# Performance work log

Hardware: AMD Instinct MI355X
Metric: run time of the kernel (lower is better)

## Reference

```python
import jax, jax.numpy as jnp
import numpy as np

N_NODES = 50000
N_EDGES = 800000
IN_C, HID_C, OUT_C = 128, 128, 64
BN_EPS = 1e-5


def setup_inputs() -> dict:
    key = jax.random.key(0)
    ks = jax.random.split(key, 12)
    def lin(k, fan_in, fan_out):
        bound = 1.0 / np.sqrt(fan_in)
        kw, kb = jax.random.split(k)
        W = jax.random.uniform(kw, (fan_in, fan_out), jnp.float32, -bound, bound)
        b = jax.random.uniform(kb, (fan_out,), jnp.float32, -bound, bound)
        return W, b
    x = jax.random.normal(ks[0], (N_NODES, IN_C), jnp.float32)
    edge_index = jax.random.randint(ks[1], (2, N_EDGES), 0, N_NODES, jnp.int32)
    w1a, b1a = lin(ks[2], IN_C, HID_C)
    w1b, b1b = lin(ks[3], HID_C, HID_C)
    w2a, b2a = lin(ks[4], HID_C, OUT_C)
    w2b, b2b = lin(ks[5], OUT_C, OUT_C)
    return {
        "x": x, "edge_index": edge_index,
        "w1a": w1a, "b1a": b1a, "g1": jnp.ones((HID_C,)), "be1": jnp.zeros((HID_C,)),
        "w1b": w1b, "b1b": b1b,
        "w2a": w2a, "b2a": b2a, "g2": jnp.ones((OUT_C,)), "be2": jnp.zeros((OUT_C,)),
        "w2b": w2b, "b2b": b2b,
    }


def _batchnorm(h, gamma, beta):
    # training-style BN over node dim, biased variance (torch BatchNorm1d)
    mean = jnp.mean(h, axis=0)
    var = jnp.mean(jnp.square(h - mean), axis=0)
    return (h - mean) * jax.lax.rsqrt(var + BN_EPS) * gamma + beta


def _gin_layer(x, src, dst, n_nodes, w_a, b_a, gamma, beta, w_b, b_b):
    # GINConv with eps=0: MLP(x + sum_{j->i} x_j)
    agg = jax.ops.segment_sum(x[src], dst, num_segments=n_nodes)  # [N, C]
    h = x + agg
    h = h @ w_a + b_a
    h = jax.nn.relu(_batchnorm(h, gamma, beta))
    return h @ w_b + b_b


def reference(x, edge_index, w1a, b1a, g1, be1, w1b, b1b, w2a, b2a, g2, be2, w2b, b2b):
    src, dst = edge_index[0], edge_index[1]
    n = x.shape[0]
    h = _gin_layer(x, src, dst, n, w1a, b1a, g1, be1, w1b, b1b)
    h = jax.nn.relu(h)  # dropout p=0.0 -> identity
    h = _gin_layer(h, src, dst, n, w2a, b2a, g2, be2, w2b, b2b)
    return jax.nn.log_softmax(h, axis=-1)
```

## Files before the change

kernel.cpp:

```cpp
#include <hip/hip_runtime.h>


typedef unsigned short u16;
typedef unsigned int u32;
typedef __attribute__((ext_vector_type(8))) short short8;
typedef __attribute__((ext_vector_type(4))) short short4v;
typedef __attribute__((ext_vector_type(4))) float f32x4;

#define DEV_INLINE __device__ __forceinline__

DEV_INLINE void atomAddF(float* p, float v) { unsafeAtomicAdd(p, v); }

DEV_INLINE u16 f2bf(float f) {
    unsigned u = __float_as_uint(f);
    u += 0x7fffu + ((u >> 16) & 1u);
    return (u16)(u >> 16);
}
DEV_INLINE float bf2f(u16 h) { return __uint_as_float(((unsigned)h) << 16); }

__global__ __launch_bounds__(256) void wprep4_k(
    const float* __restrict__ w1a, const float* __restrict__ w1b,
    const float* __restrict__ w2a, const float* __restrict__ w2b,
    short* __restrict__ o1a, short* __restrict__ o1b,
    short* __restrict__ o2a, short* __restrict__ o2b)
{
    int b = blockIdx.x;
    const float* W; short* wf; int K, NOUT;
    if (b < 8)       { W = w1a; wf = o1a; K = 128; NOUT = 128; }
    else if (b < 16) { W = w1b; wf = o1b; K = 128; NOUT = 128; b -= 8; }
    else if (b < 20) { W = w2a; wf = o2a; K = 128; NOUT = 64;  b -= 16; }
    else             { W = w2b; wf = o2b; K = 64;  NOUT = 64;  b -= 20; }
    const int u = b * 256 + threadIdx.x;
    const int units = (NOUT / 16) * (K / 32) * 64;
    if (u >= units) return;
    const int per_ct = (K / 32) * 64;
    const int ct = u / per_ct;
    const int rem = u % per_ct;
    const int kc = rem >> 6;
    const int l = rem & 63;
    const int col = ct * 16 + (l & 15);
    const int k0 = kc * 32 + (l >> 4) * 8;
    short8 pk;
#pragma unroll
    for (int j = 0; j < 8; j++)
        pk[j] = (short)f2bf(W[(size_t)(k0 + j) * NOUT + col]);
    *(short8*)&wf[(size_t)u * 8] = pk;
}

template <int KD, int NC, bool ABF16, bool BNIN, bool BIAS, bool RELUOUT,
          bool LOGSM, bool OBF16>
__global__ __launch_bounds__(256) void mgemm(
    const void* __restrict__ Ap, const short* __restrict__ Wf,
    const float* __restrict__ sc, const float* __restrict__ sh,
    const float* __restrict__ bias, void* __restrict__ outp, int M)
{
    constexpr int BM = 128;
    constexpr int KC = KD / 32;
    constexpr int CT = NC / 16;
    __shared__ short Asl[BM * KD];
    __shared__ short Bsl[NC * KD];

    const int t = threadIdx.x;
    const int l = t & 63;
    const int w = t >> 6;

    {
        const float4* src = (const float4*)Wf;
        float4* dst = (float4*)Bsl;
        constexpr int NU = NC * KD / 8;
#pragma unroll
        for (int u = t; u < NU; u += 256) dst[u] = src[u];
    }
    {
        const int r = t >> 1;
        const int half = t & 1;
        const int grow = blockIdx.x * BM + r;
        const int rt = r >> 4;
        constexpr int KH = KD / 2;
        u16 hv[KH];
        if (grow < M) {
            if constexpr (ABF16) {
                const u16* ap = (const u16*)Ap + (size_t)grow * KD + half * KH;
#pragma unroll
                for (int i = 0; i < KH / 8; i++)
                    *(short8*)&hv[i * 8] = ((const short8*)ap)[i];
                if constexpr (BNIN) {
#pragma unroll
                    for (int i = 0; i < KH; i++) {
                        const int k = half * KH + i;
                        hv[i] = f2bf(fmaxf(0.f, bf2f(hv[i]) * sc[k] + sh[k]));
                    }
                }
            } else {
                const float* ap = (const float*)Ap + (size_t)grow * KD + half * KH;
#pragma unroll
                for (int i = 0; i < KH / 4; i++) {
                    const float4 v = ((const float4*)ap)[i];
                    float f0 = v.x, f1 = v.y, f2 = v.z, f3 = v.w;
                    if constexpr (BNIN) {
                        const int k = half * KH + i * 4;
                        f0 = fmaxf(0.f, f0 * sc[k + 0] + sh[k + 0]);
                        f1 = fmaxf(0.f, f1 * sc[k + 1] + sh[k + 1]);
                        f2 = fmaxf(0.f, f2 * sc[k + 2] + sh[k + 2]);
                        f3 = fmaxf(0.f, f3 * sc[k + 3] + sh[k + 3]);
                    }
                    hv[i * 4 + 0] = f2bf(f0); hv[i * 4 + 1] = f2bf(f1);
                    hv[i * 4 + 2] = f2bf(f2); hv[i * 4 + 3] = f2bf(f3);
                }
            }
        } else {
#pragma unroll
            for (int i = 0; i < KH; i++) hv[i] = 0;
        }
#pragma unroll
        for (int g = 0; g < KH / 8; g++) {
            const int k0 = half * KH + g * 8;
            const int kc = k0 >> 5;
            const int lane = (r & 15) + ((k0 >> 3) & 3) * 16;
            *(short8*)&Asl[((rt * KC + kc) * 64 + lane) * 8] =
                *(short8*)&hv[g * 8];
        }
    }
    __syncthreads();

    const int rt0 = w * 2;
    f32x4 acc[2][CT];
#pragma unroll
    for (int i = 0; i < 2; i++)
#pragma unroll
        for (int c = 0; c < CT; c++) acc[i][c] = (f32x4){0.f, 0.f, 0.f, 0.f};

#pragma unroll
    for (int kc = 0; kc < KC; kc++) {
        const short8 x0 = *(const short8*)&Asl[((rt0 * KC + kc) * 64 + l) * 8];
        const short8 x1 = *(const short8*)&Asl[(((rt0 + 1) * KC + kc) * 64 + l) * 8];
#pragma unroll
        for (int ct = 0; ct < CT; ct++) {
            const short8 wb = *(const short8*)&Bsl[((ct * KC + kc) * 64 + l) * 8];
            acc[0][ct] = __builtin_amdgcn_mfma_f32_16x16x32_bf16(wb, x0, acc[0][ct], 0, 0, 0);
            acc[1][ct] = __builtin_amdgcn_mfma_f32_16x16x32_bf16(wb, x1, acc[1][ct], 0, 0, 0);
        }
    }

    const int cbase = (l >> 4) * 4;
#pragma unroll
    for (int rr = 0; rr < 2; rr++) {
        const int grow = blockIdx.x * BM + (rt0 + rr) * 16 + (l & 15);
        if constexpr (!LOGSM) {
            if (grow < M) {
#pragma unroll
                for (int ct = 0; ct < CT; ct++) {
                    f32x4 o = acc[rr][ct];
                    if constexpr (BIAS) {
                        const float4 bv = *(const float4*)&bias[ct * 16 + cbase];
                        o[0] += bv.x; o[1] += bv.y; o[2] += bv.z; o[3] += bv.w;
                    }
                    if constexpr (RELUOUT) {
#pragma unroll
                        for (int j = 0; j < 4; j++) o[j] = fmaxf(o[j], 0.f);
                    }
                    if constexpr (OBF16) {
                        short4v o16;
#pragma unroll
                        for (int j = 0; j < 4; j++) o16[j] = (short)f2bf(o[j]);
                        *(short4v*)&((u16*)outp)[(size_t)grow * NC + ct * 16 + cbase] = o16;
                    } else {
                        *(f32x4*)&((float*)outp)[(size_t)grow * NC + ct * 16 + cbase] = o;
                    }
                }
            }
        } else {
            float v[CT * 4];
#pragma unroll
            for (int ct = 0; ct < CT; ct++) {
                const float4 bv = *(const float4*)&bias[ct * 16 + cbase];
                v[ct * 4 + 0] = acc[rr][ct][0] + bv.x;
                v[ct * 4 + 1] = acc[rr][ct][1] + bv.y;
                v[ct * 4 + 2] = acc[rr][ct][2] + bv.z;
                v[ct * 4 + 3] = acc[rr][ct][3] + bv.w;
            }
            float m = v[0];
#pragma unroll
            for (int j = 1; j < CT * 4; j++) m = fmaxf(m, v[j]);
            m = fmaxf(m, __shfl_xor(m, 16));
            m = fmaxf(m, __shfl_xor(m, 32));
            float s = 0.f;
#pragma unroll
            for (int j = 0; j < CT * 4; j++) s += __expf(v[j] - m);
            s += __shfl_xor(s, 16);
            s += __shfl_xor(s, 32);
            const float lg = m + __logf(s);
            if (grow < M) {
#pragma unroll
                for (int ct = 0; ct < CT; ct++) {
                    f32x4 o;
#pragma unroll
                    for (int j = 0; j < 4; j++) o[j] = v[ct * 4 + j] - lg;
                    *(f32x4*)&((float*)outp)[(size_t)grow * NC + ct * 16 + cbase] = o;
                }
            }
        }
    }
}

__global__ __launch_bounds__(256) void hist_k(const int* __restrict__ ei,
                                              int* __restrict__ cnt, int E)
{
    const int gid = blockIdx.x * blockDim.x + threadIdx.x;
    const int stride = gridDim.x * blockDim.x;
    for (int e = gid; e < E; e += stride) atomicAdd(&cnt[ei[E + e]], 1);
}

__global__ __launch_bounds__(256) void bsum_k(const int* __restrict__ cnt,
                                              int* __restrict__ bsum, int N)
{
    __shared__ int ws[4];
    const int i = blockIdx.x * 256 + threadIdx.x;
    int v = (i < N) ? cnt[i] : 0;
    for (int d = 32; d; d >>= 1) v += __shfl_xor(v, d, 64);
    if ((threadIdx.x & 63) == 0) ws[threadIdx.x >> 6] = v;
    __syncthreads();
    if (threadIdx.x == 0) bsum[blockIdx.x] = ws[0] + ws[1] + ws[2] + ws[3];
}

__global__ __launch_bounds__(256) void bscan_k(const int* __restrict__ bsum,
                                               int* __restrict__ bpre, int G1)
{
    __shared__ int part[256];
    const int t = threadIdx.x;
    const int v = (t < G1) ? bsum[t] : 0;
    part[t] = v;
    __syncthreads();
    for (int d = 1; d < 256; d <<= 1) {
        const int u = (t >= d) ? part[t - d] : 0;
        __syncthreads();
        part[t] += u;
        __syncthreads();
    }
    bpre[t] = part[t] - v;
}

__global__ __launch_bounds__(256) void offs_k(const int* __restrict__ cnt,
                                              const int* __restrict__ bpre,
                                              int* __restrict__ off,
                                              int* __restrict__ cursor,
                                              int N, int E)
{
    __shared__ int part[256];
    const int t = threadIdx.x;
    const int i = blockIdx.x * 256 + t;
    const int v = (i < N) ? cnt[i] : 0;
    part[t] = v;
    __syncthreads();
    for (int d = 1; d < 256; d <<= 1) {
        const int u = (t >= d) ? part[t - d] : 0;
        __syncthreads();
        part[t] += u;
        __syncthreads();
    }
    if (i < N) {
        const int o = bpre[blockIdx.x] + part[t] - v;
        off[i] = o;
        cursor[i] = o;
    }
    if (blockIdx.x == 0 && t == 0) off[N] = E;
}

__global__ __launch_bounds__(256) void fill_k(const int* __restrict__ ei,
                                              int* __restrict__ cursor,
                                              int* __restrict__ srcs, int E)
{
    const int gid = blockIdx.x * blockDim.x + threadIdx.x;
    const int stride = gridDim.x * blockDim.x;
    for (int e = gid; e < E; e += stride) {
        const int s = ei[e];
        const int d = ei[E + e];
        const int pos = atomicAdd(&cursor[d], 1);
        srcs[pos] = s;
    }
}

template <int C>
__global__ __launch_bounds__(256) void segsum_bf(
    const u16* __restrict__ p, const int* __restrict__ off,
    const int* __restrict__ srcs, u16* __restrict__ out,
    float* __restrict__ sum, float* __restrict__ sumsq, int N)
{
    constexpr int BLKN = 8;
    constexpr int VPL = C / 64;
    __shared__ float red[4][64][2 * VPL];

    const int wv = threadIdx.x >> 6;
    const int l  = threadIdx.x & 63;
    const int base = blockIdx.x * 4 * BLKN;

    float ss[VPL], qq[VPL];
#pragma unroll
    for (int v = 0; v < VPL; v++) { ss[v] = 0.f; qq[v] = 0.f; }

    for (int i = 0; i < BLKN; i++) {
        const int n = base + i * 4 + wv;
        if (n < N) {
            const int lo = __builtin_amdgcn_readfirstlane(off[n]);
            const int hi = __builtin_amdgcn_readfirstlane(off[n + 1]);
            float acc[VPL];
            if constexpr (VPL == 2) {
                const u32 u = *(const u32*)&p[(size_t)n * C + 2 * l];
                acc[0] = bf2f((u16)u);
                acc[1] = bf2f((u16)(u >> 16));
            } else {
                acc[0] = bf2f(p[(size_t)n * C + l]);
            }
            const int cnt = hi - lo;
            if (cnt > 0) {
                const int last = hi - 1;
                int idx[8];
#pragma unroll
                for (int j = 0; j < 8; j++) idx[j] = srcs[min(lo + j, last)];
                for (int e = lo; e < hi; e += 8) {
                    int nx[8];
#pragma unroll
                    for (int j = 0; j < 8; j++)
                        nx[j] = srcs[min(e + 8 + j, last)];
#pragma unroll
                    for (int j = 0; j < 8; j++) {
                        const bool live = (e + j) < hi;
                        if constexpr (VPL == 2) {
                            const u32 u = *(const u32*)&p[(size_t)idx[j] * C + 2 * l];
                            const float v0 = bf2f((u16)u);
                            const float v1 = bf2f((u16)(u >> 16));
                            acc[0] += live ? v0 : 0.f;
                            acc[1] += live ? v1 : 0.f;
                        } else {
                            const float v = bf2f(p[(size_t)idx[j] * C + l]);
                            acc[0] += live ? v : 0.f;
                        }
                    }
#pragma unroll
                    for (int j = 0; j < 8; j++) idx[j] = nx[j];
                }
            }
            if constexpr (VPL == 2) {
                const u16 r0 = f2bf(acc[0]);
                const u16 r1 = f2bf(acc[1]);
                *(u32*)&out[(size_t)n * C + 2 * l] = (u32)r0 | ((u32)r1 << 16);
                const float f0 = bf2f(r0), f1 = bf2f(r1);
                ss[0] += f0; qq[0] += f0 * f0;
                ss[1] += f1; qq[1] += f1 * f1;
            } else {
                const u16 r = f2bf(acc[0]);
                out[(size_t)n * C + l] = r;
                const float f = bf2f(r);
                ss[0] += f; qq[0] += f * f;
            }
        }
    }

#pragma unroll
    for (int v = 0; v < VPL; v++) {
        red[wv][l][2 * v] = ss[v];
        red[wv][l][2 * v + 1] = qq[v];
    }
    __syncthreads();
    if (wv == 0) {
#pragma unroll
        for (int v = 0; v < VPL; v++) {
            float a = 0.f, b = 0.f;
#pragma unroll
            for (int w2 = 0; w2 < 4; w2++) {
                a += red[w2][l][2 * v];
                b += red[w2][l][2 * v + 1];
            }
            const int ch = (VPL == 2) ? (2 * l + v) : l;
            atomAddF(&sum[ch], a);
            atomAddF(&sumsq[ch], b);
        }
    }
}

__global__ void bnfinal_k(const float* __restrict__ sum,
                          const float* __restrict__ sumsq,
                          const float* __restrict__ g,
                          const float* __restrict__ be,
                          float* __restrict__ sc, float* __restrict__ sh,
                          int C, float invN)
{
    const int c = threadIdx.x;
    if (c < C) {
        const float m = sum[c] * invN;
        const float v = sumsq[c] * invN - m * m;
        const float r = rsqrtf(v + 1e-5f);
        const float s = g[c] * r;
        sc[c] = s;
        sh[c] = be[c] - m * s;
    }
}

extern "C" void kernel_launch(void* const* d_in, const int* in_sizes, int n_in,
                              void* d_out, int out_size, void* d_ws, size_t ws_size,
                              hipStream_t stream)
{
    const float* x   = (const float*)d_in[0];
    const int*   ei  = (const int*)d_in[1];
    const float* w1a = (const float*)d_in[2];
    const float* g1  = (const float*)d_in[4];
    const float* be1 = (const float*)d_in[5];
    const float* w1b = (const float*)d_in[6];
    const float* b1b = (const float*)d_in[7];
    const float* w2a = (const float*)d_in[8];
    const float* g2  = (const float*)d_in[10];
    const float* be2 = (const float*)d_in[11];
    const float* w2b = (const float*)d_in[12];
    const float* b2b = (const float*)d_in[13];
    float* out = (float*)d_out;

    const int N = in_sizes[0] / 128;
    const int E = in_sizes[1] / 2;

    u16* buf1 = (u16*)d_ws;
    u16* buf2 = buf1 + (size_t)N * 128;
    float* stats = (float*)(buf2 + (size_t)N * 128);
    float* sum1 = stats,       *sq1 = stats + 128;
    float* sum2 = stats + 256, *sq2 = stats + 320;
    float* sc1  = stats + 384, *sh1 = stats + 512;
    float* sc2  = stats + 640, *sh2 = stats + 704;
    int* cnt    = (int*)(stats + 1024);
    int* off    = cnt + N;
    int* cursor = off + N + 1;
    int* srcs   = cursor + N;
    int* bsum   = srcs + E;
    int* bpre   = bsum + 256;
    short* w1af = (short*)(bpre + 256);
    short* w1bf = w1af + 128 * 128;
    short* w2af = w1bf + 128 * 128;
    short* w2bf = w2af + 128 * 64;
    u16* p1 = buf1;
    u16* s1 = buf2;
    u16* h1 = buf1;
    u16* p2 = buf2;
    u16* s2 = buf2 + (size_t)N * 64;

    hipMemsetAsync(stats, 0, 1024 * sizeof(float) + (size_t)N * sizeof(int), stream);

    const int G1 = (N + 255) / 256;
    const int gb = (N + 127) / 128;
    const int gs = (N + 31) / 32;

    hist_k<<<1024, 256, 0, stream>>>(ei, cnt, E);
    bsum_k<<<G1, 256, 0, stream>>>(cnt, bsum, N);
    bscan_k<<<1, 256, 0, stream>>>(bsum, bpre, G1);
    offs_k<<<G1, 256, 0, stream>>>(cnt, bpre, off, cursor, N, E);
    fill_k<<<1024, 256, 0, stream>>>(ei, cursor, srcs, E);

    wprep4_k<<<22, 256, 0, stream>>>(w1a, w1b, w2a, w2b, w1af, w1bf, w2af, w2bf);

    mgemm<128, 128, false, false, false, false, false, true>
        <<<gb, 256, 0, stream>>>(x, w1af, nullptr, nullptr, nullptr, p1, N);
    segsum_bf<128><<<gs, 256, 0, stream>>>(p1, off, srcs, s1, sum1, sq1, N);
    bnfinal_k<<<1, 128, 0, stream>>>(sum1, sq1, g1, be1, sc1, sh1, 128, 1.f / N);
    mgemm<128, 128, true, true, true, true, false, true>
        <<<gb, 256, 0, stream>>>(s1, w1bf, sc1, sh1, b1b, h1, N);

    mgemm<128, 64, true, false, false, false, false, true>
        <<<gb, 256, 0, stream>>>(h1, w2af, nullptr, nullptr, nullptr, p2, N);
    segsum_bf<64><<<gs, 256, 0, stream>>>(p2, off, srcs, s2, sum2, sq2, N);
    bnfinal_k<<<1, 64, 0, stream>>>(sum2, sq2, g2, be2, sc2, sh2, 64, 1.f / N);
    mgemm<64, 64, true, true, true, false, true, false>
        <<<gb, 256, 0, stream>>>(s2, w2bf, sc2, sh2, b2b, out, N);
}
```

Measured before the change: 309.1 us.

## Fuse BN finalize into GEMM prologue and halve GEMM row tile

New measurement: 302.1 us. 2.3% less time.

```diff
diff --git a/kernel.cpp b/kernel.cpp
--- a/kernel.cpp
+++ b/kernel.cpp
@@ -51,18 +51,34 @@
           bool LOGSM, bool OBF16>
 __global__ __launch_bounds__(256) void mgemm(
     const void* __restrict__ Ap, const short* __restrict__ Wf,
-    const float* __restrict__ sc, const float* __restrict__ sh,
+    const float* __restrict__ sum, const float* __restrict__ sumsq,
+    const float* __restrict__ g, const float* __restrict__ be, float invN,
     const float* __restrict__ bias, void* __restrict__ outp, int M)
 {
-    constexpr int BM = 128;
+    constexpr int BM = 64;
     constexpr int KC = KD / 32;
     constexpr int CT = NC / 16;
+    constexpr int KQ = KD / 4;
     __shared__ short Asl[BM * KD];
     __shared__ short Bsl[NC * KD];
+    __shared__ float scb[BNIN ? KD : 1];
+    __shared__ float shb[BNIN ? KD : 1];
 
     const int t = threadIdx.x;
     const int l = t & 63;
     const int w = t >> 6;
+
+    if constexpr (BNIN) {
+        if (t < KD) {
+            const float m = sum[t] * invN;
+            const float v = sumsq[t] * invN - m * m;
+            const float r = rsqrtf(v + 1e-5f);
+            const float s = g[t] * r;
+            scb[t] = s;
+            shb[t] = be[t] - m * s;
+        }
+        __syncthreads();
+    }
 
     {
         const float4* src = (const float4*)Wf;
@@ -72,37 +88,36 @@
         for (int u = t; u < NU; u += 256) dst[u] = src[u];
     }
     {
-        const int r = t >> 1;
-        const int half = t & 1;
+        const int r = t >> 2;
+        const int q = t & 3;
         const int grow = blockIdx.x * BM + r;
         const int rt = r >> 4;
-        constexpr int KH = KD / 2;
-        u16 hv[KH];
+        u16 hv[KQ];
         if (grow < M) {
             if constexpr (ABF16) {
-                const u16* ap = (const u16*)Ap + (size_t)grow * KD + half * KH;
-#pragma unroll
-                for (int i = 0; i < KH / 8; i++)
+                const u16* ap = (const u16*)Ap + (size_t)grow * KD + q * KQ;
+#pragma unroll
+                for (int i = 0; i < KQ / 8; i++)
                     *(short8*)&hv[i * 8] = ((const short8*)ap)[i];
                 if constexpr (BNIN) {
 #pragma unroll
-                    for (int i = 0; i < KH; i++) {
-                        const int k = half * KH + i;
-                        hv[i] = f2bf(fmaxf(0.f, bf2f(hv[i]) * sc[k] + sh[k]));
+                    for (int i = 0; i < KQ; i++) {
+                        const int k = q * KQ + i;
+                        hv[i] = f2bf(fmaxf(0.f, bf2f(hv[i]) * scb[k] + shb[k]));
                     }
                 }
             } else {
-                const float* ap = (const float*)Ap + (size_t)grow * KD + half * KH;
-#pragma unroll
-                for (int i = 0; i < KH / 4; i++) {
+                const float* ap = (const float*)Ap + (size_t)grow * KD + q * KQ;
+#pragma unroll
+                for (int i = 0; i < KQ / 4; i++) {
                     const float4 v = ((const float4*)ap)[i];
                     float f0 = v.x, f1 = v.y, f2 = v.z, f3 = v.w;
                     if constexpr (BNIN) {
-                        const int k = half * KH + i * 4;
-                        f0 = fmaxf(0.f, f0 * sc[k + 0] + sh[k + 0]);
-                        f1 = fmaxf(0.f, f1 * sc[k + 1] + sh[k + 1]);
-                        f2 = fmaxf(0.f, f2 * sc[k + 2] + sh[k + 2]);
-                        f3 = fmaxf(0.f, f3 * sc[k + 3] + sh[k + 3]);
+                        const int k = q * KQ + i * 4;
+                        f0 = fmaxf(0.f, f0 * scb[k + 0] + shb[k + 0]);
+                        f1 = fmaxf(0.f, f1 * scb[k + 1] + shb[k + 1]);
+                        f2 = fmaxf(0.f, f2 * scb[k + 2] + shb[k + 2]);
+                        f3 = fmaxf(0.f, f3 * scb[k + 3] + shb[k + 3]);
                     }
                     hv[i * 4 + 0] = f2bf(f0); hv[i * 4 + 1] = f2bf(f1);
                     hv[i * 4 + 2] = f2bf(f2); hv[i * 4 + 3] = f2bf(f3);
@@ -110,94 +125,86 @@
             }
         } else {
 #pragma unroll
-            for (int i = 0; i < KH; i++) hv[i] = 0;
-        }
-#pragma unroll
-        for (int g = 0; g < KH / 8; g++) {
-            const int k0 = half * KH + g * 8;
+            for (int i = 0; i < KQ; i++) hv[i] = 0;
+        }
+#pragma unroll
+        for (int gg = 0; gg < KQ / 8; gg++) {
+            const int k0 = q * KQ + gg * 8;
             const int kc = k0 >> 5;
             const int lane = (r & 15) + ((k0 >> 3) & 3) * 16;
             *(short8*)&Asl[((rt * KC + kc) * 64 + lane) * 8] =
-                *(short8*)&hv[g * 8];
+                *(short8*)&hv[gg * 8];
         }
     }
     __syncthreads();
 
-    const int rt0 = w * 2;
-    f32x4 acc[2][CT];
-#pragma unroll
-    for (int i = 0; i < 2; i++)
-#pragma unroll
-        for (int c = 0; c < CT; c++) acc[i][c] = (f32x4){0.f, 0.f, 0.f, 0.f};
+    f32x4 acc[CT];
+#pragma unroll
+    for (int c = 0; c < CT; c++) acc[c] = (f32x4){0.f, 0.f, 0.f, 0.f};
 
 #pragma unroll
     for (int kc = 0; kc < KC; kc++) {
-        const short8 x0 = *(const short8*)&Asl[((rt0 * KC + kc) * 64 + l) * 8];
-        const short8 x1 = *(const short8*)&Asl[(((rt0 + 1) * KC + kc) * 64 + l) * 8];
+        const short8 x0 = *(const short8*)&Asl[((w * KC + kc) * 64 + l) * 8];
 #pragma unroll
         for (int ct = 0; ct < CT; ct++) {
             const short8 wb = *(const short8*)&Bsl[((ct * KC + kc) * 64 + l) * 8];
-            acc[0][ct] = __builtin_amdgcn_mfma_f32_16x16x32_bf16(wb, x0, acc[0][ct], 0, 0, 0);
-            acc[1][ct] = __builtin_amdgcn_mfma_f32_16x16x32_bf16(wb, x1, acc[1][ct], 0, 0, 0);
+            acc[ct] = __builtin_amdgcn_mfma_f32_16x16x32_bf16(wb, x0, acc[ct], 0, 0, 0);
         }
     }
 
     const int cbase = (l >> 4) * 4;
-#pragma unroll
-    for (int rr = 0; rr < 2; rr++) {
-        const int grow = blockIdx.x * BM + (rt0 + rr) * 16 + (l & 15);
-        if constexpr (!LOGSM) {
-            if (grow < M) {
-#pragma unroll
-                for (int ct = 0; ct < CT; ct++) {
-                    f32x4 o = acc[rr][ct];
-                    if constexpr (BIAS) {
-                        const float4 bv = *(const float4*)&bias[ct * 16 + cbase];
-                        o[0] += bv.x; o[1] += bv.y; o[2] += bv.z; o[3] += bv.w;
-                    }
-                    if constexpr (RELUOUT) {
-#pragma unroll
-                        for (int j = 0; j < 4; j++) o[j] = fmaxf(o[j], 0.f);
-                    }
-                    if constexpr (OBF16) {
-                        short4v o16;
-#pragma unroll
-                        for (int j = 0; j < 4; j++) o16[j] = (short)f2bf(o[j]);
-                        *(short4v*)&((u16*)outp)[(size_t)grow * NC + ct * 16 + cbase] = o16;
-                    } else {
-                        *(f32x4*)&((float*)outp)[(size_t)grow * NC + ct * 16 + cbase] = o;
-                    }
-                }
-            }
-        } else {
-            float v[CT * 4];
+    const int grow = blockIdx.x * BM + w * 16 + (l & 15);
+    if constexpr (!LOGSM) {
+        if (grow < M) {
 #pragma unroll
             for (int ct = 0; ct < CT; ct++) {
-                const float4 bv = *(const float4*)&bias[ct * 16 + cbase];
-                v[ct * 4 + 0] = acc[rr][ct][0] + bv.x;
-                v[ct * 4 + 1] = acc[rr][ct][1] + bv.y;
-                v[ct * 4 + 2] = acc[rr][ct][2] + bv.z;
-                v[ct * 4 + 3] = acc[rr][ct][3] + bv.w;
-            }
-            float m = v[0];
-#pragma unroll
-            for (int j = 1; j < CT * 4; j++) m = fmaxf(m, v[j]);
-            m = fmaxf(m, __shfl_xor(m, 16));
-            m = fmaxf(m, __shfl_xor(m, 32));
-            float s = 0.f;
-#pragma unroll
-            for (int j = 0; j < CT * 4; j++) s += __expf(v[j] - m);
-            s += __shfl_xor(s, 16);
-            s += __shfl_xor(s, 32);
-            const float lg = m + __logf(s);
-            if (grow < M) {
-#pragma unroll
-                for (int ct = 0; ct < CT; ct++) {
-                    f32x4 o;
-#pragma unroll
-                    for (int j = 0; j < 4; j++) o[j] = v[ct * 4 + j] - lg;
+                f32x4 o = acc[ct];
+                if constexpr (BIAS) {
+                    const float4 bv = *(const float4*)&bias[ct * 16 + cbase];
+                    o[0] += bv.x; o[1] += bv.y; o[2] += bv.z; o[3] += bv.w;
+                }
+                if constexpr (RELUOUT) {
+#pragma unroll
+                    for (int j = 0; j < 4; j++) o[j] = fmaxf(o[j], 0.f);
+                }
+                if constexpr (OBF16) {
+                    short4v o16;
+#pragma unroll
+                    for (int j = 0; j < 4; j++) o16[j] = (short)f2bf(o[j]);
+                    *(short4v*)&((u16*)outp)[(size_t)grow * NC + ct * 16 + cbase] = o16;
+                } else {
                     *(f32x4*)&((float*)outp)[(size_t)grow * NC + ct * 16 + cbase] = o;
                 }
+            }
+        }
+    } else {
+        float v[CT * 4];
+#pragma unroll
+        for (int ct = 0; ct < CT; ct++) {
+            const float4 bv = *(const float4*)&bias[ct * 16 + cbase];
+            v[ct * 4 + 0] = acc[ct][0] + bv.x;
+            v[ct * 4 + 1] = acc[ct][1] + bv.y;
+            v[ct * 4 + 2] = acc[ct][2] + bv.z;
+            v[ct * 4 + 3] = acc[ct][3] + bv.w;
+        }
+        float m = v[0];
+#pragma unroll
+        for (int j = 1; j < CT * 4; j++) m = fmaxf(m, v[j]);
+        m = fmaxf(m, __shfl_xor(m, 16));
+        m = fmaxf(m, __shfl_xor(m, 32));
+        float s = 0.f;
+#pragma unroll
+        for (int j = 0; j < CT * 4; j++) s += __expf(v[j] - m);
+        s += __shfl_xor(s, 16);
+        s += __shfl_xor(s, 32);
+        const float lg = m + __logf(s);
+        if (grow < M) {
+#pragma unroll
+            for (int ct = 0; ct < CT; ct++) {
+                f32x4 o;
+#pragma unroll
+                for (int j = 0; j < 4; j++) o[j] = v[ct * 4 + j] - lg;
+                *(f32x4*)&((float*)outp)[(size_t)grow * NC + ct * 16 + cbase] = o;
             }
         }
     }
@@ -378,24 +385,6 @@
     }
 }
 
-__global__ void bnfinal_k(const float* __restrict__ sum,
-                          const float* __restrict__ sumsq,
-                          const float* __restrict__ g,
-                          const float* __restrict__ be,
-                          float* __restrict__ sc, float* __restrict__ sh,
-                          int C, float invN)
-{
-    const int c = threadIdx.x;
-    if (c < C) {
-        const float m = sum[c] * invN;
-        const float v = sumsq[c] * invN - m * m;
-        const float r = rsqrtf(v + 1e-5f);
-        const float s = g[c] * r;
-        sc[c] = s;
-        sh[c] = be[c] - m * s;
-    }
-}
-
 extern "C" void kernel_launch(void* const* d_in, const int* in_sizes, int n_in,
                               void* d_out, int out_size, void* d_ws, size_t ws_size,
                               hipStream_t stream)
@@ -422,8 +411,6 @@
     float* stats = (float*)(buf2 + (size_t)N * 128);
     float* sum1 = stats,       *sq1 = stats + 128;
     float* sum2 = stats + 256, *sq2 = stats + 320;
-    float* sc1  = stats + 384, *sh1 = stats + 512;
-    float* sc2  = stats + 640, *sh2 = stats + 704;
     int* cnt    = (int*)(stats + 1024);
     int* off    = cnt + N;
     int* cursor = off + N + 1;
@@ -443,8 +430,9 @@
     hipMemsetAsync(stats, 0, 1024 * sizeof(float) + (size_t)N * sizeof(int), stream);
 
     const int G1 = (N + 255) / 256;
-    const int gb = (N + 127) / 128;
+    const int gb = (N + 63) / 64;
     const int gs = (N + 31) / 32;
+    const float invN = 1.f / N;
 
     hist_k<<<1024, 256, 0, stream>>>(ei, cnt, E);
     bsum_k<<<G1, 256, 0, stream>>>(cnt, bsum, N);
@@ -455,16 +443,16 @@
     wprep4_k<<<22, 256, 0, stream>>>(w1a, w1b, w2a, w2b, w1af, w1bf, w2af, w2bf);
 
     mgemm<128, 128, false, false, false, false, false, true>
-        <<<gb, 256, 0, stream>>>(x, w1af, nullptr, nullptr, nullptr, p1, N);
+        <<<gb, 256, 0, stream>>>(x, w1af, nullptr, nullptr, nullptr, nullptr,
+                                 0.f, nullptr, p1, N);
     segsum_bf<128><<<gs, 256, 0, stream>>>(p1, off, srcs, s1, sum1, sq1, N);
-    bnfinal_k<<<1, 128, 0, stream>>>(sum1, sq1, g1, be1, sc1, sh1, 128, 1.f / N);
     mgemm<128, 128, true, true, true, true, false, true>
-        <<<gb, 256, 0, stream>>>(s1, w1bf, sc1, sh1, b1b, h1, N);
+        <<<gb, 256, 0, stream>>>(s1, w1bf, sum1, sq1, g1, be1, invN, b1b, h1, N);
 
     mgemm<128, 64, true, false, false, false, false, true>
-        <<<gb, 256, 0, stream>>>(h1, w2af, nullptr, nullptr, nullptr, p2, N);
+        <<<gb, 256, 0, stream>>>(h1, w2af, nullptr, nullptr, nullptr, nullptr,
+                                 0.f, nullptr, p2, N);
     segsum_bf<64><<<gs, 256, 0, stream>>>(p2, off, srcs, s2, sum2, sq2, N);
-    bnfinal_k<<<1, 64, 0, stream>>>(sum2, sq2, g2, be2, sc2, sh2, 64, 1.f / N);
     mgemm<64, 64, true, true, true, false, true, false>
-        <<<gb, 256, 0, stream>>>(s2, w2bf, sc2, sh2, b2b, out, N);
-}
+        <<<gb, 256, 0, stream>>>(s2, w2bf, sum2, sq2, g2, be2, invN, b2b, out, N);
+}
```
